# Kernel tuning notes

Hardware: AMD Instinct MI355X
Metric: run time of the kernel (lower is better)

Reference implementation:

```python
import jax, jax.numpy as jnp
import numpy as np


def _gcn_layer(x, W, b, src, dst, norm, n_nodes):
    # PyG GCNConv: h = x @ W, then degree-normalized scatter-add over edges (incl. self loops), then + bias
    h = x @ W                                   # [N, F_out]
    msg = h[src] * norm[:, None]                # [E+N, F_out]
    out = jax.ops.segment_sum(msg, dst, num_segments=n_nodes)
    return out + b


def _norm_and_loops(edge_index, n_nodes):
    # add self loops, compute symmetric normalization deg^-1/2[src]*deg^-1/2[dst]
    loop = jnp.arange(n_nodes, dtype=edge_index.dtype)
    src = jnp.concatenate([edge_index[0], loop])
    dst = jnp.concatenate([edge_index[1], loop])
    deg = jax.ops.segment_sum(jnp.ones_like(dst, dtype=jnp.float32), dst, num_segments=n_nodes)
    dinv = jnp.where(deg > 0, jax.lax.rsqrt(deg), 0.0)
    norm = dinv[src] * dinv[dst]
    return src, dst, norm


def setup_inputs() -> dict:
    key = jax.random.key(0)
    k1, k2, k3, k4 = jax.random.split(key, 4)
    N, E, F = 100000, 1600000, 512
    x = jax.random.normal(k1, (N, F), dtype=jnp.float32)
    edge_index = jax.random.randint(k2, (2, E), 0, N, dtype=jnp.int64)
    W1 = jax.random.normal(k3, (F, 128), dtype=jnp.float32) * (1.0 / np.sqrt(F))
    b1 = jnp.zeros((128,), dtype=jnp.float32)
    W2 = jax.random.normal(k4, (128, 64), dtype=jnp.float32) * (1.0 / np.sqrt(128))
    b2 = jnp.zeros((64,), dtype=jnp.float32)
    return {"x": x, "edge_index": edge_index, "W1": W1, "b1": b1, "W2": W2, "b2": b2}


def reference(x, edge_index, W1, b1, W2, b2):
    n_nodes = x.shape[0]
    src, dst, norm = _norm_and_loops(edge_index, n_nodes)
    h = jax.nn.relu(_gcn_layer(x, W1, b1, src, dst, norm, n_nodes))
    z = jax.nn.relu(_gcn_layer(h, W2, b2, src, dst, norm, n_nodes))
    return z
```

## Files before the change

kernel.cpp:

```cpp
#include <hip/hip_runtime.h>

#define SCAN_B 1024

using bf16x8 = __attribute__((ext_vector_type(8))) short;
using f32x4  = __attribute__((ext_vector_type(4))) float;
typedef unsigned short ushort4v __attribute__((ext_vector_type(4)));
typedef _Float16 half4v __attribute__((ext_vector_type(4)));
typedef _Float16 half8v __attribute__((ext_vector_type(8)));

__device__ inline void split1(float x, unsigned short& h, unsigned short& l) {
  unsigned u  = __float_as_uint(x);
  unsigned hu = u & 0xFFFF0000u;
  float lo = x - __uint_as_float(hu);
  unsigned lu = __float_as_uint(lo);
  h = (unsigned short)(hu >> 16);
  l = (unsigned short)((lu + 0x7FFFu + ((lu >> 16) & 1u)) >> 16);
}


__global__ void zero2_kernel(int* __restrict__ a, int* __restrict__ b, int n) {
  int i = blockIdx.x * blockDim.x + threadIdx.x;
  if (i < n) { a[i] = 0; b[i] = 0; }
}

__global__ void count_kernel(const int* __restrict__ ei, int* __restrict__ cnt, int E) {
  int i = blockIdx.x * blockDim.x + threadIdx.x;
  if (i < E) atomicAdd(&cnt[ei[E + i]], 1);
}

__global__ void dinv_kernel(const int* __restrict__ cnt, float* __restrict__ dinv, int n) {
  int i = blockIdx.x * blockDim.x + threadIdx.x;
  if (i < n) dinv[i] = rsqrtf((float)(cnt[i] + 1));
}

__global__ void scan1_kernel(const int* __restrict__ cnt, int* __restrict__ rowstart,
                             int* __restrict__ bsum, int n) {
  __shared__ int sm[SCAN_B];
  const int t = threadIdx.x;
  const int i = blockIdx.x * SCAN_B + t;
  int v = (i < n) ? (cnt[i] + 1) : 0;
  sm[t] = v;
  __syncthreads();
  for (int off = 1; off < SCAN_B; off <<= 1) {
    int x = (t >= off) ? sm[t - off] : 0;
    __syncthreads();
    if (t >= off) sm[t] += x;
    __syncthreads();
  }
  if (i < n) rowstart[i] = sm[t] - v;
  if (t == SCAN_B - 1) bsum[blockIdx.x] = sm[t];
}

__global__ void scan2_kernel(int* __restrict__ bsum, int nb) {
  __shared__ int sm[SCAN_B];
  const int t = threadIdx.x;
  int v = (t < nb) ? bsum[t] : 0;
  sm[t] = v;
  __syncthreads();
  for (int off = 1; off < SCAN_B; off <<= 1) {
    int x = (t >= off) ? sm[t - off] : 0;
    __syncthreads();
    if (t >= off) sm[t] += x;
    __syncthreads();
  }
  if (t < nb) bsum[t] = sm[t] - v;
}

__global__ void scan3_kernel(int* __restrict__ rowstart, const int* __restrict__ bsum, int n) {
  int i = blockIdx.x * blockDim.x + threadIdx.x;
  if (i < n) rowstart[i] += bsum[i / SCAN_B];
}

__global__ void fill_kernel(const int* __restrict__ ei, int* __restrict__ fillc,
                            const int* __restrict__ rowstart, const float* __restrict__ dinv,
                            float2* __restrict__ ew, int E) {
  int e = blockIdx.x * blockDim.x + threadIdx.x;
  if (e < E) {
    int s = ei[e];
    int d = ei[E + e];
    int p = atomicAdd(&fillc[d], 1);
    ew[rowstart[d] + p] = make_float2(__int_as_float(s), dinv[s] * dinv[d]);
  }
}

__global__ void selfedge_kernel(const int* __restrict__ rowstart, const int* __restrict__ cnt,
                                const float* __restrict__ dinv, float2* __restrict__ ew, int N) {
  int n = blockIdx.x * blockDim.x + threadIdx.x;
  if (n < N) {
    float dn = dinv[n];
    ew[rowstart[n] + cnt[n]] = make_float2(__int_as_float(n), dn * dn);
  }
}

__global__ void wsplit_kernel(const float* __restrict__ W, unsigned short* __restrict__ Wh,
                              unsigned short* __restrict__ Wl, int K, int N) {
  int i = blockIdx.x * blockDim.x + threadIdx.x;
  if (i < K * N) {
    int k = i / N, n = i % N;
    unsigned short h, l;
    split1(W[i], h, l);
    Wh[(size_t)n * K + k] = h;
    Wl[(size_t)n * K + k] = l;
  }
}


template <int BM, int BN, typename CT>
__global__ void __launch_bounds__(512, 2)
gemm_mfma_kernel(const float* __restrict__ A, const unsigned short* __restrict__ Wh,
                 const unsigned short* __restrict__ Wl, CT* __restrict__ C,
                 int M, int K) {
  constexpr int BK   = 32;
  constexpr int LDK  = 40;
  constexpr int MR   = BM / 2 / 16;
  constexpr int NR   = BN / 4 / 16;
  constexpr int N    = BN;
  constexpr int LDC  = NR * 16 + 4;
  constexpr int SMA  = (BM + BN) * LDK * 4;
  constexpr int SME  = 8 * 16 * LDC * 4;
  constexpr int SMEM = SMA > SME ? SMA : SME;

  __shared__ __align__(16) char smem[SMEM];
  unsigned short* Ah = (unsigned short*)smem;
  unsigned short* Al = Ah + (size_t)BM * LDK;
  unsigned short* Bh = Al + (size_t)BM * LDK;
  unsigned short* Bl = Bh + (size_t)BN * LDK;

  const int tid  = threadIdx.x;
  const int lane = tid & 63;
  const int w    = tid >> 6;
  const int wm   = w >> 2;
  const int wn   = w & 3;
  const int fr   = lane & 15;
  const int fq   = lane >> 4;
  const int m0   = blockIdx.x * BM;

  const int a_c = tid & 7;
  const int a_m = tid >> 3;
  const int br  = tid >> 2;
  const int bj  = tid & 3;

  f32x4 acc[MR][NR] = {};

  for (int kt = 0; kt < K; kt += BK) {
    float4 av[2];
#pragma unroll
    for (int p = 0; p < 2; ++p) {
      const int gm = m0 + a_m + 64 * p;
      av[p] = (gm < M) ? *(const float4*)&A[(size_t)gm * K + kt + 4 * a_c]
                       : make_float4(0.f, 0.f, 0.f, 0.f);
    }
    uint4 bht, blt;
    if (tid < BN * 4) {
      bht = *(const uint4*)&Wh[(size_t)br * K + kt + 8 * bj];
      blt = *(const uint4*)&Wl[(size_t)br * K + kt + 8 * bj];
    }

    __syncthreads();

#pragma unroll
    for (int p = 0; p < 2; ++p) {
      const int r = a_m + 64 * p;
      ushort4v hv, lv;
      split1(av[p].x, ((unsigned short*)&hv)[0], ((unsigned short*)&lv)[0]);
      split1(av[p].y, ((unsigned short*)&hv)[1], ((unsigned short*)&lv)[1]);
      split1(av[p].z, ((unsigned short*)&hv)[2], ((unsigned short*)&lv)[2]);
      split1(av[p].w, ((unsigned short*)&hv)[3], ((unsigned short*)&lv)[3]);
      *(ushort4v*)((char*)Ah + r * (LDK * 2) + a_c * 8) = hv;
      *(ushort4v*)((char*)Al + r * (LDK * 2) + a_c * 8) = lv;
    }
    if (tid < BN * 4) {
      *(uint4*)((char*)Bh + br * (LDK * 2) + 16 * bj) = bht;
      *(uint4*)((char*)Bl + br * (LDK * 2) + 16 * bj) = blt;
    }
    __syncthreads();

    bf16x8 bh[NR], bl[NR];
#pragma unroll
    for (int ni = 0; ni < NR; ++ni) {
      const int r = wn * (NR * 16) + ni * 16 + fr;
      bh[ni] = *(const bf16x8*)((const char*)Bh + r * (LDK * 2) + fq * 16);
      bl[ni] = *(const bf16x8*)((const char*)Bl + r * (LDK * 2) + fq * 16);
    }
#pragma unroll
    for (int mi = 0; mi < MR; ++mi) {
      const int r = wm * 64 + mi * 16 + fr;
      bf16x8 ah = *(const bf16x8*)((const char*)Ah + r * (LDK * 2) + fq * 16);
      bf16x8 al = *(const bf16x8*)((const char*)Al + r * (LDK * 2) + fq * 16);
#pragma unroll
      for (int ni = 0; ni < NR; ++ni) {
        acc[mi][ni] = __builtin_amdgcn_mfma_f32_16x16x32_bf16(ah, bh[ni], acc[mi][ni], 0, 0, 0);
        acc[mi][ni] = __builtin_amdgcn_mfma_f32_16x16x32_bf16(ah, bl[ni], acc[mi][ni], 0, 0, 0);
        acc[mi][ni] = __builtin_amdgcn_mfma_f32_16x16x32_bf16(al, bh[ni], acc[mi][ni], 0, 0, 0);
      }
    }
  }

  __syncthreads();
  {
    float* cst = (float*)smem + (size_t)w * (16 * LDC);
    constexpr int CPR   = NR * 4;
    constexpr int EPASS = (16 * CPR + 63) / 64;
#pragma unroll
    for (int mi = 0; mi < MR; ++mi) {
#pragma unroll
      for (int ni = 0; ni < NR; ++ni)
#pragma unroll
        for (int r = 0; r < 4; ++r)
          cst[(fq * 4 + r) * LDC + ni * 16 + fr] = acc[mi][ni][r];
#pragma unroll
      for (int p = 0; p < EPASS; ++p) {
        const int idx = p * 64 + lane;
        if (idx < 16 * CPR) {
          const int row = idx / CPR;
          const int ch  = idx % CPR;
          const int gm  = m0 + wm * 64 + mi * 16 + row;
          float4 v = *(const float4*)&cst[row * LDC + ch * 4];
          if (gm < M) {
            if constexpr (sizeof(CT) == 2) {
              half4v hv = {(_Float16)v.x, (_Float16)v.y, (_Float16)v.z, (_Float16)v.w};
              *(half4v*)&C[(size_t)gm * N + wn * (NR * 16) + ch * 4] = hv;
            } else {
              *(float4*)&C[(size_t)gm * N + wn * (NR * 16) + ch * 4] = v;
            }
          }
        }
      }
    }
  }
}


template <int F>
__global__ void agg_kernel(const _Float16* __restrict__ hin, const int* __restrict__ rowstart,
                           const int* __restrict__ cnt, const float2* __restrict__ ew,
                           const float* __restrict__ bias, float* __restrict__ outp, int N) {
  constexpr int LPE = F / 8;
  constexpr int EPW = 64 / LPE;
  const int wave = (int)((blockIdx.x * (size_t)blockDim.x + threadIdx.x) >> 6);
  if (wave >= N) return;
  const int lane = threadIdx.x & 63;
  const int sub  = lane / LPE;
  const int c    = lane % LPE;
  const int n    = wave;

  const int beg = rowstart[n];
  const int end = beg + cnt[n] + 1;

  float acc[8] = {};
  int j = beg + sub;
  for (; j + 3 * EPW < end; j += 4 * EPW) {
    const float2 e0 = ew[j];
    const float2 e1 = ew[j + EPW];
    const float2 e2 = ew[j + 2 * EPW];
    const float2 e3 = ew[j + 3 * EPW];
    const half8v v0 = *(const half8v*)&hin[(size_t)__float_as_int(e0.x) * F + c * 8];
    const half8v v1 = *(const half8v*)&hin[(size_t)__float_as_int(e1.x) * F + c * 8];
    const half8v v2 = *(const half8v*)&hin[(size_t)__float_as_int(e2.x) * F + c * 8];
    const half8v v3 = *(const half8v*)&hin[(size_t)__float_as_int(e3.x) * F + c * 8];
#pragma unroll
    for (int i = 0; i < 8; ++i) {
      acc[i] = fmaf((float)v0[i], e0.y, acc[i]);
      acc[i] = fmaf((float)v1[i], e1.y, acc[i]);
      acc[i] = fmaf((float)v2[i], e2.y, acc[i]);
      acc[i] = fmaf((float)v3[i], e3.y, acc[i]);
    }
  }
  for (; j < end; j += EPW) {
    const float2 e = ew[j];
    const half8v v = *(const half8v*)&hin[(size_t)__float_as_int(e.x) * F + c * 8];
#pragma unroll
    for (int i = 0; i < 8; ++i) acc[i] = fmaf((float)v[i], e.y, acc[i]);
  }

#pragma unroll
  for (int d = LPE; d < 64; d <<= 1)
#pragma unroll
    for (int i = 0; i < 8; ++i) acc[i] += __shfl_xor(acc[i], d);

  if (lane < LPE) {
    const float4 b0 = *(const float4*)&bias[c * 8];
    const float4 b1 = *(const float4*)&bias[c * 8 + 4];
    float4 r0, r1;
    r0.x = fmaxf(acc[0] + b0.x, 0.f);
    r0.y = fmaxf(acc[1] + b0.y, 0.f);
    r0.z = fmaxf(acc[2] + b0.z, 0.f);
    r0.w = fmaxf(acc[3] + b0.w, 0.f);
    r1.x = fmaxf(acc[4] + b1.x, 0.f);
    r1.y = fmaxf(acc[5] + b1.y, 0.f);
    r1.z = fmaxf(acc[6] + b1.z, 0.f);
    r1.w = fmaxf(acc[7] + b1.w, 0.f);
    *(float4*)&outp[(size_t)n * F + c * 8] = r0;
    *(float4*)&outp[(size_t)n * F + c * 8 + 4] = r1;
  }
}


extern "C" void kernel_launch(void* const* d_in, const int* in_sizes, int n_in,
                              void* d_out, int out_size, void* d_ws, size_t ws_size,
                              hipStream_t stream) {
  const float* x  = (const float*)d_in[0];
  const int*   ei = (const int*)d_in[1];
  const float* W1 = (const float*)d_in[2];
  const float* b1 = (const float*)d_in[3];
  const float* W2 = (const float*)d_in[4];
  const float* b2 = (const float*)d_in[5];
  float* out = (float*)d_out;

  const int F1 = in_sizes[3];
  const int F2 = in_sizes[5];
  const int F0 = in_sizes[2] / F1;
  const int N  = in_sizes[0] / F0;
  const int E  = in_sizes[1] / 2;

  char* ws = (char*)d_ws;
  size_t off = 0;
  auto alloc = [&](size_t bytes) -> void* {
    void* p = ws + off;
    off = (off + bytes + 255) & ~(size_t)255;
    return p;
  };

  int*    cnt      = (int*)alloc((size_t)N * 4);
  int*    fillc    = (int*)alloc((size_t)N * 4);
  int*    rowstart = (int*)alloc((size_t)N * 4);
  float*  dinv     = (float*)alloc((size_t)N * 4);
  const int nb     = (N + SCAN_B - 1) / SCAN_B;
  int*    bsum     = (int*)alloc((size_t)nb * 4);
  float2* ew       = (float2*)alloc(((size_t)E + N) * 8);
  _Float16* h      = (_Float16*)alloc((size_t)N * F1 * 2);
  float*  h1       = (float*)alloc((size_t)N * F1 * 4);
  _Float16* h2     = h;
  unsigned short* W1h = (unsigned short*)alloc((size_t)F0 * F1 * 2);
  unsigned short* W1l = (unsigned short*)alloc((size_t)F0 * F1 * 2);
  unsigned short* W2h = (unsigned short*)alloc((size_t)F1 * F2 * 2);
  unsigned short* W2l = (unsigned short*)alloc((size_t)F1 * F2 * 2);

  zero2_kernel<<<(N + 255) / 256, 256, 0, stream>>>(cnt, fillc, N);
  count_kernel<<<(E + 255) / 256, 256, 0, stream>>>(ei, cnt, E);
  dinv_kernel<<<(N + 255) / 256, 256, 0, stream>>>(cnt, dinv, N);
  scan1_kernel<<<nb, SCAN_B, 0, stream>>>(cnt, rowstart, bsum, N);
  scan2_kernel<<<1, SCAN_B, 0, stream>>>(bsum, nb);
  scan3_kernel<<<(N + 255) / 256, 256, 0, stream>>>(rowstart, bsum, N);
  fill_kernel<<<(E + 255) / 256, 256, 0, stream>>>(ei, fillc, rowstart, dinv, ew, E);
  selfedge_kernel<<<(N + 255) / 256, 256, 0, stream>>>(rowstart, cnt, dinv, ew, N);
  wsplit_kernel<<<(F0 * F1 + 255) / 256, 256, 0, stream>>>(W1, W1h, W1l, F0, F1);
  wsplit_kernel<<<(F1 * F2 + 255) / 256, 256, 0, stream>>>(W2, W2h, W2l, F1, F2);

  gemm_mfma_kernel<128, 128, _Float16><<<(N + 127) / 128, 512, 0, stream>>>(x, W1h, W1l, h, N, F0);
  {
    const long blocks = ((long)N * 64 + 255) / 256;
    agg_kernel<128><<<(int)blocks, 256, 0, stream>>>(h, rowstart, cnt, ew, b1, h1, N);
  }

  gemm_mfma_kernel<128, 64, _Float16><<<(N + 127) / 128, 512, 0, stream>>>(h1, W2h, W2l, h2, N, F1);
  {
    const long blocks = ((long)N * 64 + 255) / 256;
    agg_kernel<64><<<(int)blocks, 256, 0, stream>>>(h2, rowstart, cnt, ew, b2, out, N);
  }
}
```

Before: 378.4 us.

## Fuse preprocessing kernels and prefetch next GEMM K-tile into registers

Folds the dinv computation into the first scan kernel, merges the edge-fill and self-loop kernels into one launch, and combines the two weight-split kernels into a single launch, cutting four kernel launches. The GEMM main loop now issues global loads for the next K tile right after the shared-memory stores, so they overlap with the MFMA work on the current tile. The prefetch keeps more live registers, which could pressure occupancy under the 512x2 launch bounds.

```diff
diff --git a/kernel.cpp b/kernel.cpp
--- a/kernel.cpp
+++ b/kernel.cpp
@@ -28,17 +28,14 @@
   if (i < E) atomicAdd(&cnt[ei[E + i]], 1);
 }
 
-__global__ void dinv_kernel(const int* __restrict__ cnt, float* __restrict__ dinv, int n) {
-  int i = blockIdx.x * blockDim.x + threadIdx.x;
-  if (i < n) dinv[i] = rsqrtf((float)(cnt[i] + 1));
-}
-
 __global__ void scan1_kernel(const int* __restrict__ cnt, int* __restrict__ rowstart,
-                             int* __restrict__ bsum, int n) {
+                             int* __restrict__ bsum, float* __restrict__ dinv, int n) {
   __shared__ int sm[SCAN_B];
   const int t = threadIdx.x;
   const int i = blockIdx.x * SCAN_B + t;
-  int v = (i < n) ? (cnt[i] + 1) : 0;
+  int c = (i < n) ? cnt[i] : 0;
+  if (i < n) dinv[i] = rsqrtf((float)(c + 1));
+  int v = (i < n) ? (c + 1) : 0;
   sm[t] = v;
   __syncthreads();
   for (int off = 1; off < SCAN_B; off <<= 1) {
@@ -71,36 +68,42 @@
   if (i < n) rowstart[i] += bsum[i / SCAN_B];
 }
 
-__global__ void fill_kernel(const int* __restrict__ ei, int* __restrict__ fillc,
-                            const int* __restrict__ rowstart, const float* __restrict__ dinv,
-                            float2* __restrict__ ew, int E) {
-  int e = blockIdx.x * blockDim.x + threadIdx.x;
-  if (e < E) {
-    int s = ei[e];
-    int d = ei[E + e];
+__global__ void fillself_kernel(const int* __restrict__ ei, int* __restrict__ fillc,
+                                const int* __restrict__ rowstart, const int* __restrict__ cnt,
+                                const float* __restrict__ dinv, float2* __restrict__ ew,
+                                int E, int N) {
+  int i = blockIdx.x * blockDim.x + threadIdx.x;
+  if (i < E) {
+    int s = ei[i];
+    int d = ei[E + i];
     int p = atomicAdd(&fillc[d], 1);
     ew[rowstart[d] + p] = make_float2(__int_as_float(s), dinv[s] * dinv[d]);
-  }
-}
-
-__global__ void selfedge_kernel(const int* __restrict__ rowstart, const int* __restrict__ cnt,
-                                const float* __restrict__ dinv, float2* __restrict__ ew, int N) {
-  int n = blockIdx.x * blockDim.x + threadIdx.x;
-  if (n < N) {
+  } else if (i < E + N) {
+    int n = i - E;
     float dn = dinv[n];
     ew[rowstart[n] + cnt[n]] = make_float2(__int_as_float(n), dn * dn);
   }
 }
 
-__global__ void wsplit_kernel(const float* __restrict__ W, unsigned short* __restrict__ Wh,
-                              unsigned short* __restrict__ Wl, int K, int N) {
-  int i = blockIdx.x * blockDim.x + threadIdx.x;
-  if (i < K * N) {
-    int k = i / N, n = i % N;
+__global__ void wsplit2_kernel(const float* __restrict__ W1, unsigned short* __restrict__ W1h,
+                               unsigned short* __restrict__ W1l, int K1, int N1,
+                               const float* __restrict__ W2, unsigned short* __restrict__ W2h,
+                               unsigned short* __restrict__ W2l, int K2, int N2) {
+  int i = blockIdx.x * blockDim.x + threadIdx.x;
+  const int n1 = K1 * N1;
+  if (i < n1) {
+    int k = i / N1, n = i % N1;
     unsigned short h, l;
-    split1(W[i], h, l);
-    Wh[(size_t)n * K + k] = h;
-    Wl[(size_t)n * K + k] = l;
+    split1(W1[i], h, l);
+    W1h[(size_t)n * K1 + k] = h;
+    W1l[(size_t)n * K1 + k] = l;
+  } else if (i < n1 + K2 * N2) {
+    int j = i - n1;
+    int k = j / N2, n = j % N2;
+    unsigned short h, l;
+    split1(W2[j], h, l);
+    W2h[(size_t)n * K2 + k] = h;
+    W2l[(size_t)n * K2 + k] = l;
   }
 }
 
@@ -140,22 +143,30 @@
   const int br  = tid >> 2;
   const int bj  = tid & 3;
 
-  f32x4 acc[MR][NR] = {};
-
-  for (int kt = 0; kt < K; kt += BK) {
-    float4 av[2];
+  float4 av[2];
+  uint4  bht, blt;
+
+  auto loadA = [&](int kt) {
 #pragma unroll
     for (int p = 0; p < 2; ++p) {
       const int gm = m0 + a_m + 64 * p;
       av[p] = (gm < M) ? *(const float4*)&A[(size_t)gm * K + kt + 4 * a_c]
                        : make_float4(0.f, 0.f, 0.f, 0.f);
     }
-    uint4 bht, blt;
+  };
+  auto loadB = [&](int kt) {
     if (tid < BN * 4) {
       bht = *(const uint4*)&Wh[(size_t)br * K + kt + 8 * bj];
       blt = *(const uint4*)&Wl[(size_t)br * K + kt + 8 * bj];
     }
-
+  };
+
+  f32x4 acc[MR][NR] = {};
+
+  loadA(0);
+  loadB(0);
+
+  for (int kt = 0; kt < K; kt += BK) {
     __syncthreads();
 
 #pragma unroll
@@ -174,6 +185,11 @@
       *(uint4*)((char*)Bl + br * (LDK * 2) + 16 * bj) = blt;
     }
     __syncthreads();
+
+    if (kt + BK < K) {
+      loadA(kt + BK);
+      loadB(kt + BK);
+    }
 
     bf16x8 bh[NR], bl[NR];
 #pragma unroll
@@ -338,14 +354,12 @@
 
   zero2_kernel<<<(N + 255) / 256, 256, 0, stream>>>(cnt, fillc, N);
   count_kernel<<<(E + 255) / 256, 256, 0, stream>>>(ei, cnt, E);
-  dinv_kernel<<<(N + 255) / 256, 256, 0, stream>>>(cnt, dinv, N);
-  scan1_kernel<<<nb, SCAN_B, 0, stream>>>(cnt, rowstart, bsum, N);
+  scan1_kernel<<<nb, SCAN_B, 0, stream>>>(cnt, rowstart, bsum, dinv, N);
   scan2_kernel<<<1, SCAN_B, 0, stream>>>(bsum, nb);
   scan3_kernel<<<(N + 255) / 256, 256, 0, stream>>>(rowstart, bsum, N);
-  fill_kernel<<<(E + 255) / 256, 256, 0, stream>>>(ei, fillc, rowstart, dinv, ew, E);
-  selfedge_kernel<<<(N + 255) / 256, 256, 0, stream>>>(rowstart, cnt, dinv, ew, N);
-  wsplit_kernel<<<(F0 * F1 + 255) / 256, 256, 0, stream>>>(W1, W1h, W1l, F0, F1);
-  wsplit_kernel<<<(F1 * F2 + 255) / 256, 256, 0, stream>>>(W2, W2h, W2l, F1, F2);
+  fillself_kernel<<<(E + N + 255) / 256, 256, 0, stream>>>(ei, fillc, rowstart, cnt, dinv, ew, E, N);
+  wsplit2_kernel<<<(F0 * F1 + F1 * F2 + 255) / 256, 256, 0, stream>>>(
+      W1, W1h, W1l, F0, F1, W2, W2h, W2l, F1, F2);
 
   gemm_mfma_kernel<128, 128, _Float16><<<(N + 127) / 128, 512, 0, stream>>>(x, W1h, W1l, h, N, F0);
   {
```

New measurement: 374.8 us. About the same (-1.0%).
